# Kernel tuning notes

Hardware: AMD Instinct MI355X
Metric: run time of the kernel (lower is better)

The kernel has to match this reference:

```python
import jax, jax.numpy as jnp
import numpy as np

B, T, DIM = 2, 2048, 2048
H, HKV = 16, 4
D = DIM // H          # head_dim = 128
G = H // HKV          # GQA group = 4
ROPE_BASE = 10000.0
TRAIN_SEQ_LEN = 1024  # Rotary default; T > this triggers NTK base rescale


def _rope_tables():
    # Faithful to Rotary.forward: NTK scaling when seq_len > train_seq_len.
    if T > TRAIN_SEQ_LEN:
        sc = T / TRAIN_SEQ_LEN
        base = ROPE_BASE * sc ** (D / (D - 2))
    else:
        base = ROPE_BASE
    inv = 1.0 / base ** (np.arange(0, D, 2, dtype=np.float32) / D)  # [D/2]
    f = np.outer(np.arange(T, dtype=np.float32), inv)               # [T, D/2]
    cos = jnp.asarray(np.cos(f), jnp.float32)[None, :, None, :]     # [1,T,1,D/2]
    sin = jnp.asarray(np.sin(f), jnp.float32)[None, :, None, :]
    return cos, sin


def _rms_norm(x):
    # F.rms_norm with no weight: x / sqrt(mean(x^2) + eps), eps = finfo(dtype).eps
    eps = jnp.finfo(x.dtype).eps
    return x * jax.lax.rsqrt(jnp.mean(x * x, axis=-1, keepdims=True) + eps)


def _apply_rope(x, cos, sin):
    x1, x2 = jnp.split(x, 2, axis=-1)
    return jnp.concatenate([x1 * cos + x2 * sin, -x1 * sin + x2 * cos], axis=-1)


def setup_inputs() -> dict:
    key = jax.random.key(0)
    kx, kq, kk, kv, kp = jax.random.split(key, 5)
    s = lambda fan_in: 1.0 / np.sqrt(fan_in)
    kv_dim = HKV * D
    return {
        "x": jax.random.normal(kx, (B, T, DIM), jnp.float32),
        "Wq": jax.random.normal(kq, (DIM, DIM), jnp.float32) * s(DIM),
        "Wk": jax.random.normal(kk, (kv_dim, DIM), jnp.float32) * s(DIM),
        "Wv": jax.random.normal(kv, (kv_dim, DIM), jnp.float32) * s(DIM),
        "Wproj": jax.random.normal(kp, (DIM, DIM), jnp.float32) * s(DIM),
        "q_gain": jnp.full((H,), 1.0, jnp.float32),
    }


def reference(x, Wq, Wk, Wv, Wproj, q_gain):
    # QKV projections (bias-free linears)
    q = (x @ Wq.T).reshape(B, T, H, D)
    k = (x @ Wk.T).reshape(B, T, HKV, D)
    v = (x @ Wv.T).reshape(B, T, HKV, D)

    # QK RMSNorm + RoPE + per-head q gain
    q = _rms_norm(q)
    k = _rms_norm(k)
    cos, sin = _rope_tables()
    q = _apply_rope(q, cos, sin)
    k = _apply_rope(k, cos, sin)
    q = q * q_gain[None, None, :, None]

    # GQA causal SDPA without materializing repeated K/V:
    # group query heads by kv head: q -> [B,T,HKV,G,D]
    qg = q.reshape(B, T, HKV, G, D)
    scores = jnp.einsum('btkgd,bskd->bkgts', qg, k) / np.sqrt(D)  # [B,HKV,G,T,T]
    causal = jnp.tril(jnp.ones((T, T), bool))
    scores = jnp.where(causal[None, None, None], scores, -jnp.inf)
    p = jax.nn.softmax(scores, axis=-1)
    y = jnp.einsum('bkgts,bskd->btkgd', p, v).reshape(B, T, H, D)

    out = y.reshape(B, T, DIM) @ Wproj.T
    return out, v
```

## Files before the change

### kernel.cpp

```cpp
#include <hip/hip_runtime.h>
#include <hip/hip_bf16.h>

typedef __bf16 bf16_t;
typedef __bf16 bf16x4 __attribute__((ext_vector_type(4)));
typedef __bf16 bf16x8 __attribute__((ext_vector_type(8)));
typedef float f32x4 __attribute__((ext_vector_type(4)));

#define B_    2
#define T_    2048
#define DIM_  2048
#define H_    16
#define HKV_  4
#define D_    128
#define KVDIM_ 512

__device__ __forceinline__ bf16x8 cvt8(f32x4 a, f32x4 b) {
  bf16x8 r;
  r[0] = (bf16_t)a[0]; r[1] = (bf16_t)a[1]; r[2] = (bf16_t)a[2]; r[3] = (bf16_t)a[3];
  r[4] = (bf16_t)b[0]; r[5] = (bf16_t)b[1]; r[6] = (bf16_t)b[2]; r[7] = (bf16_t)b[3];
  return r;
}
__device__ __forceinline__ bf16x4 cvt4(f32x4 a) {
  bf16x4 r;
  r[0] = (bf16_t)a[0]; r[1] = (bf16_t)a[1]; r[2] = (bf16_t)a[2]; r[3] = (bf16_t)a[3];
  return r;
}
__device__ __forceinline__ void g2l16(const void* g, void* l) {
  __builtin_amdgcn_global_load_lds(
      (const __attribute__((address_space(1))) unsigned int*)g,
      (__attribute__((address_space(3))) unsigned int*)l, 16, 0, 0);
}

__global__ __launch_bounds__(256)
void cvt_all(const float* __restrict__ x,  const float* __restrict__ wq,
             const float* __restrict__ wk, const float* __restrict__ wv,
             const float* __restrict__ wp, bf16_t* __restrict__ xb,
             bf16_t* __restrict__ wqkvb, bf16_t* __restrict__ wpb) {
  int blk = blockIdx.x;
  const float* s; bf16_t* d; int lb;
  if (blk < 4096)      { s = x;  d = xb;                              lb = blk; }
  else if (blk < 6144) { s = wq; d = wqkvb;                           lb = blk - 4096; }
  else if (blk < 6656) { s = wk; d = wqkvb + (size_t)2048 * DIM_;     lb = blk - 6144; }
  else if (blk < 7168) { s = wv; d = wqkvb + (size_t)2560 * DIM_;     lb = blk - 6656; }
  else                 { s = wp; d = wpb;                             lb = blk - 7168; }
  size_t i = (size_t)lb * 2048 + (size_t)threadIdx.x * 8;
  f32x4 a = *(const f32x4*)(s + i);
  f32x4 b = *(const f32x4*)(s + i + 4);
  *(bf16x8*)(d + i) = cvt8(a, b);
}

template <int MODE, bool AASYNC, bool WASYNC>
__global__ __launch_bounds__(256)
void gemm128(const void* __restrict__ Ag, const void* __restrict__ Wg,
             const void* __restrict__ Wg2, void* __restrict__ Cb,
             bf16_t* __restrict__ Kb, bf16_t* __restrict__ Vb,
             float* __restrict__ Vf, int M, int N, int K) {
  constexpr int LDA = AASYNC ? 32 : 40;
  constexpr int LDW = WASYNC ? 32 : 40;
  __shared__ bf16_t As[128 * LDA];
  __shared__ bf16_t Ws[128 * LDW];
  const int tid  = threadIdx.x;
  const int wave = tid >> 6, lane = tid & 63;
  const int l16  = lane & 15, lg = lane >> 4;
  const int m0 = blockIdx.y * 128, n0 = blockIdx.x * 128;
  const int wm = (wave & 1) * 64, wn = (wave >> 1) * 64;
  f32x4 acc[4][4] = {};

  for (int k0 = 0; k0 < K; k0 += 32) {
    __syncthreads();
    if constexpr (AASYNC) {
      const bf16_t* A = (const bf16_t*)Ag;
      const int r = lane >> 2, c8 = (lane & 3) * 8;
      g2l16(&A[(size_t)(m0 + wave * 32 + r) * K + k0 + c8],      &As[(wave * 32) * LDA]);
      g2l16(&A[(size_t)(m0 + wave * 32 + 16 + r) * K + k0 + c8], &As[(wave * 32 + 16) * LDA]);
    } else {
      const float* A = (const float*)Ag;
#pragma unroll
      for (int j = 0; j < 4; j++) {
        int row = wave * 32 + j * 8 + (lane >> 3);
        int cf  = (lane & 7) * 4;
        f32x4 v = *(const f32x4*)&A[(size_t)(m0 + row) * K + k0 + cf];
        *(bf16x4*)&As[row * LDA + cf] = cvt4(v);
      }
    }
    if constexpr (WASYNC) {
      const bf16_t* W = (const bf16_t*)Wg;
      const int r = lane >> 2, c8 = (lane & 3) * 8;
      g2l16(&W[(size_t)(n0 + wave * 32 + r) * K + k0 + c8],      &Ws[(wave * 32) * LDW]);
      g2l16(&W[(size_t)(n0 + wave * 32 + 16 + r) * K + k0 + c8], &Ws[(wave * 32 + 16) * LDW]);
    } else {
      const float* W;
      int nb;
      if constexpr (MODE == 3) {
        if (n0 < 512) { W = (const float*)Wg;  nb = n0; }
        else          { W = (const float*)Wg2; nb = n0 - 512; }
      } else { W = (const float*)Wg; nb = n0; }
#pragma unroll
      for (int j = 0; j < 4; j++) {
        int row = wave * 32 + j * 8 + (lane >> 3);
        int cf  = (lane & 7) * 4;
        f32x4 v = *(const f32x4*)&W[(size_t)(nb + row) * K + k0 + cf];
        *(bf16x4*)&Ws[row * LDW + cf] = cvt4(v);
      }
    }
    __syncthreads();
    bf16x8 af[4], bfr[4];
#pragma unroll
    for (int i = 0; i < 4; i++)
      af[i] = *(const bf16x8*)&As[(wm + i * 16 + l16) * LDA + lg * 8];
#pragma unroll
    for (int j = 0; j < 4; j++)
      bfr[j] = *(const bf16x8*)&Ws[(wn + j * 16 + l16) * LDW + lg * 8];
#pragma unroll
    for (int i = 0; i < 4; i++)
#pragma unroll
      for (int j = 0; j < 4; j++)
        acc[i][j] = __builtin_amdgcn_mfma_f32_16x16x32_bf16(af[i], bfr[j], acc[i][j], 0, 0, 0);
  }
#pragma unroll
  for (int i = 0; i < 4; i++)
#pragma unroll
    for (int j = 0; j < 4; j++) {
      int row = m0 + wm + i * 16 + lg * 4;
      int col = n0 + wn + j * 16 + l16;
#pragma unroll
      for (int r = 0; r < 4; r++) {
        float v = acc[i][j][r];
        if constexpr (MODE == 0) {
          ((bf16_t*)Cb)[(size_t)(row + r) * N + col] = (bf16_t)v;
        } else if constexpr (MODE == 2) {
          ((float*)Cb)[(size_t)(row + r) * N + col] = v;
        } else if constexpr (MODE == 1) {
          if (col < 2048)      ((bf16_t*)Cb)[(size_t)(row + r) * 2048 + col] = (bf16_t)v;
          else if (col < 2560) Kb[(size_t)(row + r) * 512 + (col - 2048)] = (bf16_t)v;
          else {
            int c = col - 2560;
            Vb[(size_t)(row + r) * 512 + c] = (bf16_t)v;
            Vf[(size_t)(row + r) * 512 + c] = v;
          }
        } else {
          if (col < 512) ((bf16_t*)Cb)[(size_t)(row + r) * 512 + col] = (bf16_t)v;
          else {
            int c = col - 512;
            Vb[(size_t)(row + r) * 512 + c] = (bf16_t)v;
            Vf[(size_t)(row + r) * 512 + c] = v;
          }
        }
      }
    }
}

__global__ __launch_bounds__(256)
void qk_norm_rope(bf16_t* __restrict__ Qp, bf16_t* __restrict__ Kp,
                  const float* __restrict__ gain) {
  const int lane = threadIdx.x & 63;
  int row = blockIdx.x * 4 + (threadIdx.x >> 6);
  bf16_t* Xp; int nh; bool ag;
  const int MQ = B_ * T_ * H_;
  if (row < MQ) { Xp = Qp; nh = H_;  ag = true; }
  else          { Xp = Kp; nh = HKV_; ag = false; row -= MQ; }
  const int h = row % nh;
  const int t = (row / nh) % T_;
  bf16_t* p = Xp + (size_t)row * D_;
  float x0 = (float)p[lane * 2 + 0];
  float x1 = (float)p[lane * 2 + 1];
  float ss = x0 * x0 + x1 * x1;
#pragma unroll
  for (int m = 32; m >= 1; m >>= 1) ss += __shfl_xor(ss, m);
  const float rn = rsqrtf(ss * (1.0f / 128.0f) + 1.1920929e-07f);
  x0 *= rn; x1 *= rn;
  const float y0 = __shfl_xor(x0, 32);
  const float y1 = __shfl_xor(x1, 32);
  const int i0 = (lane & 31) * 2;
  const float kfreq = -0.22349352180347601f;
  float s0, c0, s1, c1;
  float a0 = (float)t * exp2f(kfreq * (float)i0);
  float a1 = (float)t * exp2f(kfreq * (float)(i0 + 1));
  sincosf(a0, &s0, &c0);
  sincosf(a1, &s1, &c1);
  float o0, o1;
  if (lane < 32) { o0 = x0 * c0 + y0 * s0;  o1 = x1 * c1 + y1 * s1; }
  else           { o0 = x0 * c0 - y0 * s0;  o1 = x1 * c1 - y1 * s1; }
  if (ag) { float g = gain[h]; o0 *= g; o1 *= g; }
  p[lane * 2 + 0] = (bf16_t)o0;
  p[lane * 2 + 1] = (bf16_t)o1;
}

#define KLD 136
#define VLD 72
#define PLD 68

__global__ __launch_bounds__(256, 2)
void flash_attn(const bf16_t* __restrict__ Q, const bf16_t* __restrict__ Kg,
                const bf16_t* __restrict__ V, bf16_t* __restrict__ Y) {
  __shared__ bf16_t Ks[64 * KLD];
  __shared__ bf16_t Vs[D_ * VLD];
  __shared__ float  Ps[4][16 * PLD];
  const int tid  = threadIdx.x;
  const int wave = tid >> 6, lane = tid & 63;
  const int l16  = lane & 15, lg = lane >> 4;
  const int b = blockIdx.z, h = blockIdx.y;
  const int pi = blockIdx.x;
  const int hk = h >> 2;

  int qr[2];
  qr[0] = 64 * pi + 16 * wave;
  qr[1] = 64 * (31 - pi) + 16 * wave;

  bf16x8 qf[2][4];
#pragma unroll
  for (int mt = 0; mt < 2; mt++)
#pragma unroll
    for (int kk = 0; kk < 4; kk++)
      qf[mt][kk] = *(const bf16x8*)&Q[(((size_t)b * T_ + qr[mt] + l16) * H_ + h) * D_ + kk * 32 + lg * 8];

  f32x4 o[2][8] = {};
  float lsum[2][4] = {};
  const float C = 0.12752531f;

  const int sr = tid >> 4, sc = (tid & 15) * 8;
  const int sp2 = (tid & 31) * 2;
  const int dvh = (tid >> 5) * 8;

  bf16x8 kreg[4];
  bf16x8 vreg[2][2];
  auto pf_load = [&](int k0) {
#pragma unroll
    for (int j = 0; j < 4; j++)
      kreg[j] = *(const bf16x8*)&Kg[(((size_t)b * T_ + k0 + sr + 16 * j) * HKV_ + hk) * D_ + sc];
#pragma unroll
    for (int it = 0; it < 2; it++) {
      const bf16_t* vb = &V[(((size_t)b * T_ + k0 + sp2) * HKV_ + hk) * D_ + dvh + it * 64];
      vreg[it][0] = *(const bf16x8*)vb;
      vreg[it][1] = *(const bf16x8*)(vb + HKV_ * D_);
    }
  };
  auto pf_store = [&]() {
#pragma unroll
    for (int j = 0; j < 4; j++)
      *(bf16x8*)&Ks[(sr + 16 * j) * KLD + sc] = kreg[j];
#pragma unroll
    for (int it = 0; it < 2; it++) {
      int dd = dvh + it * 64;
      const unsigned short* au = (const unsigned short*)&vreg[it][0];
      const unsigned short* bu = (const unsigned short*)&vreg[it][1];
#pragma unroll
      for (int i = 0; i < 8; i++) {
        unsigned int pr = (unsigned int)au[i] | ((unsigned int)bu[i] << 16);
        *(unsigned int*)&Vs[(dd + i) * VLD + sp2] = pr;
      }
    }
  };

  const int nkb = 32 - pi;
  pf_load(0);
  for (int kb = 0; kb < nkb; kb++) {
    const int k0 = kb * 64;
    __syncthreads();
    pf_store();
    __syncthreads();
    if (kb + 1 < nkb) pf_load(k0 + 64);

    const bool act0 = (kb <= pi);

    f32x4 s[2][4] = {};
#pragma unroll
    for (int kk = 0; kk < 4; kk++) {
      bf16x8 kf[4];
#pragma unroll
      for (int f = 0; f < 4; f++)
        kf[f] = *(const bf16x8*)&Ks[(f * 16 + l16) * KLD + kk * 32 + lg * 8];
      if (act0)
#pragma unroll
        for (int f = 0; f < 4; f++)
          s[0][f] = __builtin_amdgcn_mfma_f32_16x16x32_bf16(qf[0][kk], kf[f], s[0][f], 0, 0, 0);
#pragma unroll
      for (int f = 0; f < 4; f++)
        s[1][f] = __builtin_amdgcn_mfma_f32_16x16x32_bf16(qf[1][kk], kf[f], s[1][f], 0, 0, 0);
    }
    bf16x8 pf[2][2];
    float* pw = Ps[wave];
#pragma unroll
    for (int mt = 0; mt < 2; mt++) {
      if (mt == 0 && !act0) continue;
      const bool diag = (mt == 0) ? (kb == pi) : (kb == nkb - 1);
      if (diag) {
        const int myq = qr[mt] + lg * 4;
#pragma unroll
        for (int f = 0; f < 4; f++)
#pragma unroll
          for (int r = 0; r < 4; r++) {
            int kcol = k0 + f * 16 + l16;
            float p = (kcol <= myq + r) ? exp2f(s[mt][f][r] * C) : 0.0f;
            lsum[mt][r] += p;
            pw[(lg * 4 + r) * PLD + f * 16 + l16] = p;
          }
      } else {
#pragma unroll
        for (int f = 0; f < 4; f++)
#pragma unroll
          for (int r = 0; r < 4; r++) {
            float p = exp2f(s[mt][f][r] * C);
            lsum[mt][r] += p;
            pw[(lg * 4 + r) * PLD + f * 16 + l16] = p;
          }
      }
      __threadfence_block();
      f32x4 pa0 = *(const f32x4*)&pw[l16 * PLD + lg * 8];
      f32x4 pa1 = *(const f32x4*)&pw[l16 * PLD + lg * 8 + 4];
      f32x4 pb0 = *(const f32x4*)&pw[l16 * PLD + 32 + lg * 8];
      f32x4 pb1 = *(const f32x4*)&pw[l16 * PLD + 32 + lg * 8 + 4];
      pf[mt][0] = cvt8(pa0, pa1);
      pf[mt][1] = cvt8(pb0, pb1);
      __threadfence_block();
    }
#pragma unroll
    for (int f = 0; f < 8; f++) {
      bf16x8 v0 = *(const bf16x8*)&Vs[(f * 16 + l16) * VLD + lg * 8];
      bf16x8 v1 = *(const bf16x8*)&Vs[(f * 16 + l16) * VLD + 32 + lg * 8];
      if (act0) {
        o[0][f] = __builtin_amdgcn_mfma_f32_16x16x32_bf16(pf[0][0], v0, o[0][f], 0, 0, 0);
        o[0][f] = __builtin_amdgcn_mfma_f32_16x16x32_bf16(pf[0][1], v1, o[0][f], 0, 0, 0);
      }
      o[1][f] = __builtin_amdgcn_mfma_f32_16x16x32_bf16(pf[1][0], v0, o[1][f], 0, 0, 0);
      o[1][f] = __builtin_amdgcn_mfma_f32_16x16x32_bf16(pf[1][1], v1, o[1][f], 0, 0, 0);
    }
  }
#pragma unroll
  for (int mt = 0; mt < 2; mt++) {
    float rl[4];
#pragma unroll
    for (int r = 0; r < 4; r++) {
      float l = lsum[mt][r];
      l += __shfl_xor(l, 1);
      l += __shfl_xor(l, 2);
      l += __shfl_xor(l, 4);
      l += __shfl_xor(l, 8);
      rl[r] = 1.0f / l;
    }
#pragma unroll
    for (int f = 0; f < 8; f++)
#pragma unroll
      for (int r = 0; r < 4; r++) {
        int t = qr[mt] + lg * 4 + r;
        Y[(((size_t)b * T_ + t) * H_ + h) * D_ + f * 16 + l16] = (bf16_t)(o[mt][f][r] * rl[r]);
      }
  }
}

extern "C" void kernel_launch(void* const* d_in, const int* in_sizes, int n_in,
                              void* d_out, int out_size, void* d_ws, size_t ws_size,
                              hipStream_t stream) {
  (void)in_sizes; (void)n_in; (void)out_size;
  const float* x     = (const float*)d_in[0];
  const float* Wq    = (const float*)d_in[1];
  const float* Wk    = (const float*)d_in[2];
  const float* Wv    = (const float*)d_in[3];
  const float* Wproj = (const float*)d_in[4];
  const float* qgain = (const float*)d_in[5];

  float* out  = (float*)d_out;
  float* vout = out + (size_t)B_ * T_ * DIM_;

  const size_t M = (size_t)B_ * T_;
  char* ws = (char*)d_ws;
  size_t off = 0;
  auto take = [&](size_t elems) { bf16_t* p = (bf16_t*)(ws + off); off += elems * sizeof(bf16_t); return p; };

  bf16_t* Qp = take(M * DIM_);
  bf16_t* Kp = take(M * KVDIM_);
  bf16_t* Vb = take(M * KVDIM_);

  const size_t cvt_elems = M * DIM_ + (size_t)3072 * DIM_ + (size_t)DIM_ * DIM_;
  const bool fast = (ws_size >= off + cvt_elems * sizeof(bf16_t));

  dim3 blk(256);
  if (fast) {
    bf16_t* xb     = take(M * DIM_);
    bf16_t* Wqkvb  = take((size_t)3072 * DIM_);
    bf16_t* Wpb    = take((size_t)DIM_ * DIM_);

    cvt_all<<<dim3(9216), blk, 0, stream>>>(x, Wq, Wk, Wv, Wproj, xb, Wqkvb, Wpb);

    gemm128<1, true, true><<<dim3(3072 / 128, M / 128), blk, 0, stream>>>(
        xb, Wqkvb, nullptr, Qp, Kp, Vb, vout, M, 3072, DIM_);

    qk_norm_rope<<<dim3((unsigned)((M * H_ + M * HKV_) / 4)), blk, 0, stream>>>(Qp, Kp, qgain);
    flash_attn<<<dim3(16, H_, B_), blk, 0, stream>>>(Qp, Kp, Vb, Qp);

    gemm128<2, true, true><<<dim3(DIM_ / 128, M / 128), blk, 0, stream>>>(
        Qp, Wpb, nullptr, out, nullptr, nullptr, nullptr, M, DIM_, DIM_);
  } else {
    gemm128<0, false, false><<<dim3(DIM_ / 128, M / 128), blk, 0, stream>>>(
        x, Wq, nullptr, Qp, nullptr, nullptr, nullptr, M, DIM_, DIM_);
    gemm128<3, false, false><<<dim3(2 * KVDIM_ / 128, M / 128), blk, 0, stream>>>(
        x, Wk, Wv, Kp, nullptr, Vb, vout, M, 2 * KVDIM_, DIM_);
    qk_norm_rope<<<dim3((unsigned)((M * H_ + M * HKV_) / 4)), blk, 0, stream>>>(Qp, Kp, qgain);
    flash_attn<<<dim3(16, H_, B_), blk, 0, stream>>>(Qp, Kp, Vb, Qp);
    gemm128<2, true, false><<<dim3(DIM_ / 128, M / 128), blk, 0, stream>>>(
        Qp, Wproj, nullptr, out, nullptr, nullptr, nullptr, M, DIM_, DIM_);
  }
}
```

Baseline: 337.1 us.

## Split flash-attn paired query tiles into separate blocks; specialize GEMM K at compile time

Flash attention previously had each block process a pair of query tiles (pi and 31-pi) to balance causal work. It now launches one block per 64-row query tile with a 32-wide grid. Each block holds fewer registers, and launch bounds are raised to allow 3 blocks per CU, trading explicit load balancing for more parallelism and occupancy. The GEMM kernel now takes K as a template constant, hoists its global/LDS pointer arithmetic out of the loop, and unrolls the k-loop by 2 to cut address overhead.

```diff
diff --git a/kernel.cpp b/kernel.cpp
--- a/kernel.cpp
+++ b/kernel.cpp
@@ -49,12 +49,12 @@
   *(bf16x8*)(d + i) = cvt8(a, b);
 }
 
-template <int MODE, bool AASYNC, bool WASYNC>
+template <int MODE, bool AASYNC, bool WASYNC, int KK>
 __global__ __launch_bounds__(256)
 void gemm128(const void* __restrict__ Ag, const void* __restrict__ Wg,
              const void* __restrict__ Wg2, void* __restrict__ Cb,
              bf16_t* __restrict__ Kb, bf16_t* __restrict__ Vb,
-             float* __restrict__ Vf, int M, int N, int K) {
+             float* __restrict__ Vf, int M, int N) {
   constexpr int LDA = AASYNC ? 32 : 40;
   constexpr int LDW = WASYNC ? 32 : 40;
   __shared__ bf16_t As[128 * LDA];
@@ -66,28 +66,35 @@
   const int wm = (wave & 1) * 64, wn = (wave >> 1) * 64;
   f32x4 acc[4][4] = {};
 
-  for (int k0 = 0; k0 < K; k0 += 32) {
+  const int r4 = lane >> 2, c8 = (lane & 3) * 8;
+  const bf16_t* ap0 = (const bf16_t*)Ag + (size_t)(m0 + wave * 32 + r4) * KK + c8;
+  const bf16_t* ap1 = ap0 + (size_t)16 * KK;
+  const bf16_t* wpa = (const bf16_t*)Wg + (size_t)(n0 + wave * 32 + r4) * KK + c8;
+  const bf16_t* wpb2 = wpa + (size_t)16 * KK;
+  bf16_t* lda0 = &As[(wave * 32) * LDA];
+  bf16_t* lda1 = &As[(wave * 32 + 16) * LDA];
+  bf16_t* ldw0 = &Ws[(wave * 32) * LDW];
+  bf16_t* ldw1 = &Ws[(wave * 32 + 16) * LDW];
+
+#pragma unroll 2
+  for (int k0 = 0; k0 < KK; k0 += 32) {
     __syncthreads();
     if constexpr (AASYNC) {
-      const bf16_t* A = (const bf16_t*)Ag;
-      const int r = lane >> 2, c8 = (lane & 3) * 8;
-      g2l16(&A[(size_t)(m0 + wave * 32 + r) * K + k0 + c8],      &As[(wave * 32) * LDA]);
-      g2l16(&A[(size_t)(m0 + wave * 32 + 16 + r) * K + k0 + c8], &As[(wave * 32 + 16) * LDA]);
+      g2l16(ap0 + k0, lda0);
+      g2l16(ap1 + k0, lda1);
     } else {
       const float* A = (const float*)Ag;
 #pragma unroll
       for (int j = 0; j < 4; j++) {
         int row = wave * 32 + j * 8 + (lane >> 3);
         int cf  = (lane & 7) * 4;
-        f32x4 v = *(const f32x4*)&A[(size_t)(m0 + row) * K + k0 + cf];
+        f32x4 v = *(const f32x4*)&A[(size_t)(m0 + row) * KK + k0 + cf];
         *(bf16x4*)&As[row * LDA + cf] = cvt4(v);
       }
     }
     if constexpr (WASYNC) {
-      const bf16_t* W = (const bf16_t*)Wg;
-      const int r = lane >> 2, c8 = (lane & 3) * 8;
-      g2l16(&W[(size_t)(n0 + wave * 32 + r) * K + k0 + c8],      &Ws[(wave * 32) * LDW]);
-      g2l16(&W[(size_t)(n0 + wave * 32 + 16 + r) * K + k0 + c8], &Ws[(wave * 32 + 16) * LDW]);
+      g2l16(wpa + k0, ldw0);
+      g2l16(wpb2 + k0, ldw1);
     } else {
       const float* W;
       int nb;
@@ -99,7 +106,7 @@
       for (int j = 0; j < 4; j++) {
         int row = wave * 32 + j * 8 + (lane >> 3);
         int cf  = (lane & 7) * 4;
-        f32x4 v = *(const f32x4*)&W[(size_t)(nb + row) * K + k0 + cf];
+        f32x4 v = *(const f32x4*)&W[(size_t)(nb + row) * KK + k0 + cf];
         *(bf16x4*)&Ws[row * LDW + cf] = cvt4(v);
       }
     }
@@ -190,7 +197,7 @@
 #define VLD 72
 #define PLD 68
 
-__global__ __launch_bounds__(256, 2)
+__global__ __launch_bounds__(256, 3)
 void flash_attn(const bf16_t* __restrict__ Q, const bf16_t* __restrict__ Kg,
                 const bf16_t* __restrict__ V, bf16_t* __restrict__ Y) {
   __shared__ bf16_t Ks[64 * KLD];
@@ -200,22 +207,17 @@
   const int wave = tid >> 6, lane = tid & 63;
   const int l16  = lane & 15, lg = lane >> 4;
   const int b = blockIdx.z, h = blockIdx.y;
-  const int pi = blockIdx.x;
+  const int ti = blockIdx.x;
   const int hk = h >> 2;
-
-  int qr[2];
-  qr[0] = 64 * pi + 16 * wave;
-  qr[1] = 64 * (31 - pi) + 16 * wave;
-
-  bf16x8 qf[2][4];
-#pragma unroll
-  for (int mt = 0; mt < 2; mt++)
-#pragma unroll
-    for (int kk = 0; kk < 4; kk++)
-      qf[mt][kk] = *(const bf16x8*)&Q[(((size_t)b * T_ + qr[mt] + l16) * H_ + h) * D_ + kk * 32 + lg * 8];
-
-  f32x4 o[2][8] = {};
-  float lsum[2][4] = {};
+  const int qrow = 64 * ti + 16 * wave;
+
+  bf16x8 qf[4];
+#pragma unroll
+  for (int kk = 0; kk < 4; kk++)
+    qf[kk] = *(const bf16x8*)&Q[(((size_t)b * T_ + qrow + l16) * H_ + h) * D_ + kk * 32 + lg * 8];
+
+  f32x4 o[8] = {};
+  float lsum[4] = {};
   const float C = 0.12752531f;
 
   const int sr = tid >> 4, sc = (tid & 15) * 8;
@@ -252,7 +254,7 @@
     }
   };
 
-  const int nkb = 32 - pi;
+  const int nkb = ti + 1;
   pf_load(0);
   for (int kb = 0; kb < nkb; kb++) {
     const int k0 = kb * 64;
@@ -261,91 +263,72 @@
     __syncthreads();
     if (kb + 1 < nkb) pf_load(k0 + 64);
 
-    const bool act0 = (kb <= pi);
-
-    f32x4 s[2][4] = {};
+    f32x4 s[4] = {};
 #pragma unroll
     for (int kk = 0; kk < 4; kk++) {
       bf16x8 kf[4];
 #pragma unroll
       for (int f = 0; f < 4; f++)
         kf[f] = *(const bf16x8*)&Ks[(f * 16 + l16) * KLD + kk * 32 + lg * 8];
-      if (act0)
-#pragma unroll
-        for (int f = 0; f < 4; f++)
-          s[0][f] = __builtin_amdgcn_mfma_f32_16x16x32_bf16(qf[0][kk], kf[f], s[0][f], 0, 0, 0);
 #pragma unroll
       for (int f = 0; f < 4; f++)
-        s[1][f] = __builtin_amdgcn_mfma_f32_16x16x32_bf16(qf[1][kk], kf[f], s[1][f], 0, 0, 0);
-    }
-    bf16x8 pf[2][2];
+        s[f] = __builtin_amdgcn_mfma_f32_16x16x32_bf16(qf[kk], kf[f], s[f], 0, 0, 0);
+    }
     float* pw = Ps[wave];
-#pragma unroll
-    for (int mt = 0; mt < 2; mt++) {
-      if (mt == 0 && !act0) continue;
-      const bool diag = (mt == 0) ? (kb == pi) : (kb == nkb - 1);
-      if (diag) {
-        const int myq = qr[mt] + lg * 4;
-#pragma unroll
-        for (int f = 0; f < 4; f++)
-#pragma unroll
-          for (int r = 0; r < 4; r++) {
-            int kcol = k0 + f * 16 + l16;
-            float p = (kcol <= myq + r) ? exp2f(s[mt][f][r] * C) : 0.0f;
-            lsum[mt][r] += p;
-            pw[(lg * 4 + r) * PLD + f * 16 + l16] = p;
-          }
-      } else {
-#pragma unroll
-        for (int f = 0; f < 4; f++)
-#pragma unroll
-          for (int r = 0; r < 4; r++) {
-            float p = exp2f(s[mt][f][r] * C);
-            lsum[mt][r] += p;
-            pw[(lg * 4 + r) * PLD + f * 16 + l16] = p;
-          }
-      }
-      __threadfence_block();
-      f32x4 pa0 = *(const f32x4*)&pw[l16 * PLD + lg * 8];
-      f32x4 pa1 = *(const f32x4*)&pw[l16 * PLD + lg * 8 + 4];
-      f32x4 pb0 = *(const f32x4*)&pw[l16 * PLD + 32 + lg * 8];
-      f32x4 pb1 = *(const f32x4*)&pw[l16 * PLD + 32 + lg * 8 + 4];
-      pf[mt][0] = cvt8(pa0, pa1);
-      pf[mt][1] = cvt8(pb0, pb1);
-      __threadfence_block();
-    }
+    if (kb == nkb - 1) {
+      const int myq = qrow + lg * 4;
+#pragma unroll
+      for (int f = 0; f < 4; f++)
+#pragma unroll
+        for (int r = 0; r < 4; r++) {
+          int kcol = k0 + f * 16 + l16;
+          float p = (kcol <= myq + r) ? exp2f(s[f][r] * C) : 0.0f;
+          lsum[r] += p;
+          pw[(lg * 4 + r) * PLD + f * 16 + l16] = p;
+        }
+    } else {
+#pragma unroll
+      for (int f = 0; f < 4; f++)
+#pragma unroll
+        for (int r = 0; r < 4; r++) {
+          float p = exp2f(s[f][r] * C);
+          lsum[r] += p;
+          pw[(lg * 4 + r) * PLD + f * 16 + l16] = p;
+        }
+    }
+    __threadfence_block();
+    f32x4 pa0 = *(const f32x4*)&pw[l16 * PLD + lg * 8];
+    f32x4 pa1 = *(const f32x4*)&pw[l16 * PLD + lg * 8 + 4];
+    f32x4 pb0 = *(const f32x4*)&pw[l16 * PLD + 32 + lg * 8];
+    f32x4 pb1 = *(const f32x4*)&pw[l16 * PLD + 32 + lg * 8 + 4];
+    bf16x8 pfr0 = cvt8(pa0, pa1);
+    bf16x8 pfr1 = cvt8(pb0, pb1);
+    __threadfence_block();
 #pragma unroll
     for (int f = 0; f < 8; f++) {
       bf16x8 v0 = *(const bf16x8*)&Vs[(f * 16 + l16) * VLD + lg * 8];
       bf16x8 v1 = *(const bf16x8*)&Vs[(f * 16 + l16) * VLD + 32 + lg * 8];
-      if (act0) {
-        o[0][f] = __builtin_amdgcn_mfma_f32_16x16x32_bf16(pf[0][0], v0, o[0][f], 0, 0, 0);
-        o[0][f] = __builtin_amdgcn_mfma_f32_16x16x32_bf16(pf[0][1], v1, o[0][f], 0, 0, 0);
-      }
-      o[1][f] = __builtin_amdgcn_mfma_f32_16x16x32_bf16(pf[1][0], v0, o[1][f], 0, 0, 0);
-      o[1][f] = __builtin_amdgcn_mfma_f32_16x16x32_bf16(pf[1][1], v1, o[1][f], 0, 0, 0);
+      o[f] = __builtin_amdgcn_mfma_f32_16x16x32_bf16(pfr0, v0, o[f], 0, 0, 0);
+      o[f] = __builtin_amdgcn_mfma_f32_16x16x32_bf16(pfr1, v1, o[f], 0, 0, 0);
     }
   }
-#pragma unroll
-  for (int mt = 0; mt < 2; mt++) {
-    float rl[4];
+  float rl[4];
+#pragma unroll
+  for (int r = 0; r < 4; r++) {
+    float l = lsum[r];
+    l += __shfl_xor(l, 1);
+    l += __shfl_xor(l, 2);
+    l += __shfl_xor(l, 4);
+    l += __shfl_xor(l, 8);
+    rl[r] = 1.0f / l;
+  }
+#pragma unroll
+  for (int f = 0; f < 8; f++)
 #pragma unroll
     for (int r = 0; r < 4; r++) {
-      float l = lsum[mt][r];
-      l += __shfl_xor(l, 1);
-      l += __shfl_xor(l, 2);
-      l += __shfl_xor(l, 4);
-      l += __shfl_xor(l, 8);
-      rl[r] = 1.0f / l;
-    }
-#pragma unroll
-    for (int f = 0; f < 8; f++)
-#pragma unroll
-      for (int r = 0; r < 4; r++) {
-        int t = qr[mt] + lg * 4 + r;
-        Y[(((size_t)b * T_ + t) * H_ + h) * D_ + f * 16 + l16] = (bf16_t)(o[mt][f][r] * rl[r]);
-      }
-  }
+      int t = qrow + lg * 4 + r;
+      Y[(((size_t)b * T_ + t) * H_ + h) * D_ + f * 16 + l16] = (bf16_t)(o[f][r] * rl[r]);
+    }
 }
 
 extern "C" void kernel_launch(void* const* d_in, const int* in_sizes, int n_in,
@@ -382,22 +365,22 @@
 
     cvt_all<<<dim3(9216), blk, 0, stream>>>(x, Wq, Wk, Wv, Wproj, xb, Wqkvb, Wpb);
 
-    gemm128<1, true, true><<<dim3(3072 / 128, M / 128), blk, 0, stream>>>(
-        xb, Wqkvb, nullptr, Qp, Kp, Vb, vout, M, 3072, DIM_);
+    gemm128<1, true, true, DIM_><<<dim3(3072 / 128, M / 128), blk, 0, stream>>>(
+        xb, Wqkvb, nullptr, Qp, Kp, Vb, vout, M, 3072);
 
     qk_norm_rope<<<dim3((unsigned)((M * H_ + M * HKV_) / 4)), blk, 0, stream>>>(Qp, Kp, qgain);
-    flash_attn<<<dim3(16, H_, B_), blk, 0, stream>>>(Qp, Kp, Vb, Qp);
-
-    gemm128<2, true, true><<<dim3(DIM_ / 128, M / 128), blk, 0, stream>>>(
-        Qp, Wpb, nullptr, out, nullptr, nullptr, nullptr, M, DIM_, DIM_);
+    flash_attn<<<dim3(32, H_, B_), blk, 0, stream>>>(Qp, Kp, Vb, Qp);
+
+    gemm128<2, true, true, DIM_><<<dim3(DIM_ / 128, M / 128), blk, 0, stream>>>(
+        Qp, Wpb, nullptr, out, nullptr, nullptr, nullptr, M, DIM_);
   } else {
-    gemm128<0, false, false><<<dim3(DIM_ / 128, M / 128), blk, 0, stream>>>(
-        x, Wq, nullptr, Qp, nullptr, nullptr, nullptr, M, DIM_, DIM_);
-    gemm128<3, false, false><<<dim3(2 * KVDIM_ / 128, M / 128), blk, 0, stream>>>(
-        x, Wk, Wv, Kp, nullptr, Vb, vout, M, 2 * KVDIM_, DIM_);
+    gemm128<0, false, false, DIM_><<<dim3(DIM_ / 128, M / 128), blk, 0, stream>>>(
+        x, Wq, nullptr, Qp, nullptr, nullptr, nullptr, M, DIM_);
+    gemm128<3, false, false, DIM_><<<dim3(2 * KVDIM_ / 128, M / 128), blk, 0, stream>>>(
+        x, Wk, Wv, Kp, nullptr, Vb, vout, M, 2 * KVDIM_);
     qk_norm_rope<<<dim3((unsigned)((M * H_ + M * HKV_) / 4)), blk, 0, stream>>>(Qp, Kp, qgain);
-    flash_attn<<<dim3(16, H_, B_), blk, 0, stream>>>(Qp, Kp, Vb, Qp);
-    gemm128<2, true, false><<<dim3(DIM_ / 128, M / 128), blk, 0, stream>>>(
-        Qp, Wproj, nullptr, out, nullptr, nullptr, nullptr, M, DIM_, DIM_);
+    flash_attn<<<dim3(32, H_, B_), blk, 0, stream>>>(Qp, Kp, Vb, Qp);
+    gemm128<2, true, false, DIM_><<<dim3(DIM_ / 128, M / 128), blk, 0, stream>>>(
+        Qp, Wproj, nullptr, out, nullptr, nullptr, nullptr, M, DIM_);
   }
 }
```

Result: slower. 408.2 us (+21.1%).
